# Performance work log

Hardware: AMD Instinct MI355X
Metric: run time of the kernel (lower is better)

The kernel has to match this reference:

```python
import jax, jax.numpy as jnp
import numpy as np

H = 8            # kv heads
R = 2            # qhead_ratio -> hq = 16 query heads
D = 128          # head_size
DEG = 2          # power degree
GATE_OFFSET = 6.906768  # ~log(999), gates start near 1


def setup_inputs() -> dict:
    key = jax.random.key(0)
    ks = jax.random.split(key, 7)
    B, T, C = 1, 2048, 2048
    q_dim = H * R * D   # 2048
    kv_dim = H * D      # 1024
    s = 0.02
    return {
        "hidden_states": jax.random.normal(ks[0], (B, T, C), dtype=jnp.float32),
        "Wq": jax.random.normal(ks[1], (C, q_dim), dtype=jnp.float32) * s,
        "Wk": jax.random.normal(ks[2], (C, kv_dim), dtype=jnp.float32) * s,
        "Wv": jax.random.normal(ks[3], (C, kv_dim), dtype=jnp.float32) * s,
        "Wg": jax.random.normal(ks[4], (C, H), dtype=jnp.float32) * s,
        "Wc": jax.random.normal(ks[5], (q_dim, C), dtype=jnp.float32) * s,
        "bc": jnp.zeros((C,), dtype=jnp.float32),
    }


def _power_attention(q, k, v, log_g):
    # q: [B,T,hq,D], k/v: [B,T,H,D], log_g: [B,T,H]
    B, T, hq, d = q.shape
    scale = 1.0 / d ** 0.5
    # GQA: query head i uses kv head i // R (q was viewed as (B,T,H,R,D))
    k = jnp.repeat(k, R, axis=2)            # [B,T,hq,D]
    v = jnp.repeat(v, R, axis=2)            # [B,T,hq,D]
    logG = jnp.cumsum(log_g, axis=1)        # [B,T,H]
    logG = jnp.repeat(logG, R, axis=2)      # [B,T,hq]
    logG = jnp.transpose(logG, (0, 2, 1))   # [B,hq,T]
    qk = jnp.einsum('bthd,bshd->bhts', q, k) * scale   # [B,hq,T,T]
    a = qk ** DEG                                       # even degree -> >= 0
    # gating decay exp(logG_t - logG_s) <= 1 for s <= t
    gate = logG[:, :, :, None] - logG[:, :, None, :]    # [B,hq,T,T]
    causal = jnp.tril(jnp.ones((T, T), dtype=bool))
    a = jnp.where(causal, a * jnp.exp(gate), 0.0)
    norm = jnp.sum(a, axis=-1) + 1e-6                   # [B,hq,T]
    y = jnp.einsum('bhts,bshd->bthd', a, v)             # [B,T,hq,D]
    y = y / jnp.transpose(norm, (0, 2, 1))[..., None]
    return y


def reference(hidden_states, Wq, Wk, Wv, Wg, Wc, bc):
    B, T, C = hidden_states.shape
    q = (hidden_states @ Wq).reshape(B, T, H * R, D)
    k = (hidden_states @ Wk).reshape(B, T, H, D)
    v = (hidden_states @ Wv).reshape(B, T, H, D)
    g = hidden_states @ Wg                              # [B,T,H]
    log_g = jax.nn.log_sigmoid(GATE_OFFSET + g.astype(jnp.float32))
    y = _power_attention(q, k, v, log_g)                # [B,T,hq,D]
    y = y.reshape(B, T, H * R * D)
    return y @ Wc + bc
```

## Files before the change

### kernel.cpp

```cpp
#include <hip/hip_runtime.h>

typedef unsigned short u16;
typedef unsigned int u32;
typedef unsigned long long u64;
typedef __bf16 bf16x8 __attribute__((ext_vector_type(8)));
typedef float f32x4 __attribute__((ext_vector_type(4)));

union FragAB {
  bf16x8 v;
  u16 u[8];
  u32 w[4];
  u64 d2[2];
};

__device__ __forceinline__ u16 f2bf(float f) {
  u32 u = __builtin_bit_cast(u32, f);
  u += 0x7fffu + ((u >> 16) & 1u);
  return (u16)(u >> 16);
}

__device__ __forceinline__ void gload_lds16(const void* g, void* l) {
  __builtin_amdgcn_global_load_lds((__attribute__((address_space(1))) void*)g,
                                   (__attribute__((address_space(3))) void*)l, 16, 0, 0);
}

__device__ __forceinline__ int permcol(int n) {
  int k = n & 31;
  return (n & ~31) | ((k & 12) << 1) | ((k & 16) >> 2) | (k & 3);
}

__global__ __launch_bounds__(256) void conv_perm_kernel(const float* __restrict__ in,
                                                        u16* __restrict__ out, int n4) {
  int i = blockIdx.x * 256 + threadIdx.x;
  if (i >= n4) return;
  float4 v = ((const float4*)in)[i];
  u64 pk = (u64)f2bf(v.x) | ((u64)f2bf(v.y) << 16) | ((u64)f2bf(v.z) << 32) |
           ((u64)f2bf(v.w) << 48);
  int col = (i << 2) & 2047;
  int g = (col >> 2) & 7;
  int ncol = (col & ~31) | ((2 * (g & 3) + (g >> 2)) << 2);
  size_t row = (size_t)(i >> 9);
  *(u64*)&out[row * 2048 + ncol] = pk;
}

__global__ __launch_bounds__(256) void tconv_kernel(const float* __restrict__ in,
                                                    u16* __restrict__ out, int K, int N) {
  __shared__ float tile[32][33];
  int col = threadIdx.x & 31;
  int row0 = threadIdx.x >> 5;
  int kb = blockIdx.y * 32, nb = blockIdx.x * 32;
  int pcol = permcol(col);
#pragma unroll
  for (int i = 0; i < 4; i++) {
    int r = row0 + i * 8;
    tile[r][col] = in[(size_t)(kb + r) * N + nb + col];
  }
  __syncthreads();
#pragma unroll
  for (int i = 0; i < 4; i++) {
    int r = row0 + i * 8;
    out[(size_t)(nb + r) * K + kb + pcol] = f2bf(tile[col][r]);
  }
}

__global__ __launch_bounds__(256) void tconv3_kernel(const float* __restrict__ Wq,
                                                     const float* __restrict__ Wk,
                                                     const float* __restrict__ Wv,
                                                     u16* __restrict__ slab) {
  __shared__ float tile[32][33];
  const int z = blockIdx.z;
  const float* src = (z < 2) ? Wq : (z == 2 ? Wk : Wv);
  const int srcN = (z < 2) ? 2048 : 1024;
  const int colBase = (z == 1) ? 1024 : 0;
  const int dstRowBase = z * 1024;
  int col = threadIdx.x & 31;
  int row0 = threadIdx.x >> 5;
  int kb = blockIdx.y * 32, nb = blockIdx.x * 32;
  int pcol = permcol(col);
#pragma unroll
  for (int i = 0; i < 4; i++) {
    int r = row0 + i * 8;
    tile[r][col] = src[(size_t)(kb + r) * srcN + colBase + nb + col];
  }
  __syncthreads();
#pragma unroll
  for (int i = 0; i < 4; i++) {
    int r = row0 + i * 8;
    slab[(size_t)(dstRowBase + nb + r) * 2048 + kb + pcol] = f2bf(tile[col][r]);
  }
}

__global__ __launch_bounds__(256) void gate_kernel(const float* __restrict__ hs,
                                                   const float* __restrict__ Wg,
                                                   float* __restrict__ lgt) {
  int lane = threadIdx.x & 63, wid = threadIdx.x >> 6;
  int t = blockIdx.x * 4 + wid;
  float acc[8] = {0.f, 0.f, 0.f, 0.f, 0.f, 0.f, 0.f, 0.f};
  for (int c = lane; c < 2048; c += 64) {
    float x = hs[(size_t)t * 2048 + c];
    float4 w0 = *(const float4*)&Wg[c * 8];
    float4 w1 = *(const float4*)&Wg[c * 8 + 4];
    acc[0] += x * w0.x; acc[1] += x * w0.y; acc[2] += x * w0.z; acc[3] += x * w0.w;
    acc[4] += x * w1.x; acc[5] += x * w1.y; acc[6] += x * w1.z; acc[7] += x * w1.w;
  }
#pragma unroll
  for (int h = 0; h < 8; h++) {
    float v = acc[h];
    for (int m = 1; m < 64; m <<= 1) v += __shfl_xor(v, m, 64);
    if (lane == 0) {
      float x = 6.906768f + v;
      lgt[h * 2048 + t] = -log1pf(__expf(-x));
    }
  }
}

__global__ __launch_bounds__(256) void cumsum_kernel(const float* __restrict__ lgt,
                                                     float* __restrict__ logG) {
  int h = blockIdx.x;
  __shared__ float buf[2048];
  for (int i = threadIdx.x; i < 2048; i += 256) buf[i] = lgt[h * 2048 + i];
  __syncthreads();
  for (int off = 1; off < 2048; off <<= 1) {
    float tmp[8];
#pragma unroll
    for (int j = 0; j < 8; j++) {
      int i = threadIdx.x + j * 256;
      tmp[j] = (i >= off) ? buf[i - off] : 0.f;
    }
    __syncthreads();
#pragma unroll
    for (int j = 0; j < 8; j++) {
      int i = threadIdx.x + j * 256;
      buf[i] += tmp[j];
    }
    __syncthreads();
  }
  for (int i = threadIdx.x; i < 2048; i += 256) logG[h * 2048 + i] = buf[i];
}

template <int MODE, int NT>
__global__ __launch_bounds__(512, 4) void gemm_v2(const u16* __restrict__ A,
                                                  const u16* __restrict__ BT,
                                                  void* __restrict__ C0,
                                                  void* __restrict__ C1,
                                                  int permLim) {
  __shared__ __align__(16) u16 As[2 * 128 * 64];
  __shared__ __align__(16) u16 Bs[2 * 128 * 64];
  constexpr int nwg = 16 * NT * (MODE == 2 ? 2 : 1);
  constexpr int cpx = nwg >> 3;
  const int raw = (int)blockIdx.x;
  const int wg = (raw & 7) * cpx + (raw >> 3);
  int bx, by, z;
  if constexpr (MODE == 2) {
    z = wg & 1;
    int t = wg >> 1;
    by = t >> 4;
    bx = t & 15;
  } else {
    z = 0;
    by = wg >> 4;
    bx = wg & 15;
  }
  const int kBeg = (MODE == 2) ? z * 1024 : 0;
  const int kEnd = (MODE == 2) ? kBeg + 1024 : 2048;
  constexpr int N = NT * 128;

  const int tid = threadIdx.x;
  const int lane = tid & 63, wid = tid >> 6;
  const int m0 = bx * 128, n0 = by * 128;
  const int wr = wid >> 2, wc = wid & 3;
  const int l15 = lane & 15, kg = lane >> 4;

  f32x4 acc[4][2];
#pragma unroll
  for (int i = 0; i < 4; i++)
#pragma unroll
    for (int j = 0; j < 2; j++) acc[i][j] = f32x4{0.f, 0.f, 0.f, 0.f};

  const int c0 = (wid * 2) * 64 + lane;
  const int c1 = c0 + 64;
  const int r0 = c0 >> 3, s0u = (c0 & 7) ^ (r0 & 7);
  const int r1 = c1 >> 3, s1u = (c1 & 7) ^ (r1 & 7);
  const u16* Asrc0 = A + (size_t)(m0 + r0) * 2048 + s0u * 8;
  const u16* Asrc1 = A + (size_t)(m0 + r1) * 2048 + s1u * 8;
  const u16* Bsrc0 = BT + (size_t)(n0 + r0) * 2048 + s0u * 8;
  const u16* Bsrc1 = BT + (size_t)(n0 + r1) * 2048 + s1u * 8;

  auto stage = [&](int buf, int k0) {
    u16* Ad = As + buf * 8192 + (wid * 2) * 512;
    u16* Bd = Bs + buf * 8192 + (wid * 2) * 512;
    gload_lds16(Asrc0 + k0, Ad);
    gload_lds16(Asrc1 + k0, Ad + 512);
    gload_lds16(Bsrc0 + k0, Bd);
    gload_lds16(Bsrc1 + k0, Bd + 512);
  };

  stage(0, kBeg);
  __syncthreads();

  int cur = 0;
  for (int k0 = kBeg; k0 < kEnd; k0 += 64) {
    if (k0 + 64 < kEnd) stage(cur ^ 1, k0 + 64);
    const u16* Ab = As + cur * 8192;
    const u16* Bb = Bs + cur * 8192;
#pragma unroll
    for (int ks = 0; ks < 2; ks++) {
      FragAB af[4], bfr[2];
#pragma unroll
      for (int mt = 0; mt < 4; mt++) {
        int row = wr * 64 + mt * 16 + l15;
        af[mt].v = *(const bf16x8*)&Ab[row * 64 + 8 * ((ks * 4 + kg) ^ (row & 7))];
      }
#pragma unroll
      for (int nt = 0; nt < 2; nt++) {
        int row = wc * 32 + nt * 16 + l15;
        bfr[nt].v = *(const bf16x8*)&Bb[row * 64 + 8 * ((ks * 4 + kg) ^ (row & 7))];
      }
#pragma unroll
      for (int mt = 0; mt < 4; mt++)
#pragma unroll
        for (int nt = 0; nt < 2; nt++)
          acc[mt][nt] = __builtin_amdgcn_mfma_f32_16x16x32_bf16(af[mt].v, bfr[nt].v, acc[mt][nt], 0, 0, 0);
    }
    __syncthreads();
    cur ^= 1;
  }

#pragma unroll
  for (int mt = 0; mt < 4; mt++) {
#pragma unroll
    for (int re = 0; re < 4; re++) {
      int m = m0 + wr * 64 + mt * 16 + kg * 4 + re;
#pragma unroll
      for (int nt = 0; nt < 2; nt++) {
        int n = n0 + wc * 32 + nt * 16 + l15;
        float v = acc[mt][nt][re];
        if constexpr (MODE == 2) {
          float* P = z ? (float*)C1 : (float*)C0;
          P[(size_t)m * N + n] = v;
        } else {
          int nw = (n < permLim) ? permcol(n) : n;
          ((u16*)C0)[(size_t)m * N + nw] = f2bf(v);
        }
      }
    }
  }
}

__global__ __launch_bounds__(256, 2) void power_attn(const u16* __restrict__ QKV,
                                                     const float* __restrict__ logG,
                                                     float* __restrict__ y0p,
                                                     float* __restrict__ y1p,
                                                     float* __restrict__ npart) {
  __shared__ __align__(16) u16 Ks[2 * 64 * 128];
  __shared__ __align__(16) u16 Vt[2 * 128 * 64];
  __shared__ float eS[2 * 64];

  const int raw = (int)blockIdx.x;
  const int orig = (raw & 7) * 64 + (raw >> 3);
  const int hq = orig >> 5;
  const int j_ = orig & 31;
  const int half = j_ & 1;
  const int bslot = j_ >> 1;
  const int qa = (bslot + (hq >> 1) * 3) & 15;
  const int qt = (hq & 1) ? (15 - qa) : qa;
  const int hk = hq >> 1;
  const int t0 = qt * 128;

  const int tid = threadIdx.x, lane = tid & 63, wid = tid >> 6;
  const int l15 = lane & 15, kg = lane >> 4;
  const int l7 = l15 & 7;

  const int s4 = tid & 15, dgrp = tid >> 4;
  const int ubase = 4 * (s4 >> 3) + (s4 & 3);
  const int vhb = (s4 >> 2) & 1;

  const u16* Kbase = QKV + 2048 + hk * 128;
  const u16* Vbase = QKV + 3072 + hk * 128 + dgrp * 8;
  const float* lgh = logG + hk * 2048;

  FragAB qf[2][4];
  float celg[2];
  int myT[2];
  const float scale2 = 0.0078125f;
#pragma unroll
  for (int cg = 0; cg < 2; cg++) {
    myT[cg] = t0 + wid * 16 + cg * 64 + l15;
    const u16* qrow = QKV + (size_t)myT[cg] * 4096 + hq * 128;
#pragma unroll
    for (int ks = 0; ks < 4; ks++) qf[cg][ks].v = *(const bf16x8*)(qrow + ks * 32 + kg * 8);
    celg[cg] = scale2 * __expf(lgh[myT[cg]]);
  }

  f32x4 yacc[8][2];
#pragma unroll
  for (int i = 0; i < 8; i++)
#pragma unroll
    for (int c = 0; c < 2; c++) yacc[i][c] = f32x4{0.f, 0.f, 0.f, 0.f};
  float nacc[2] = {0.f, 0.f};

  const int itBeg = half ? (qt + 1) : 0;
  const int itEnd = half ? (2 * qt + 2) : (qt + 1);

  auto stageK = [&](int s0, int bb) {
#pragma unroll
    for (int c = 0; c < 4; c++) {
      int ch = (wid * 4 + c) * 64 + lane;
      int row = ch >> 4, du = ch & 15;
      int su = du ^ (row & 7);
      gload_lds16(Kbase + (size_t)(s0 + row) * 4096 + su * 8, &Ks[bb * 8192 + (wid * 4 + c) * 512]);
    }
  };
  auto loadV = [&](int s0, uint4* vr) {
#pragma unroll
    for (int r = 0; r < 4; r++) vr[r] = *(const uint4*)(Vbase + (size_t)(s0 + 4 * s4 + r) * 4096);
  };
  auto writeV = [&](int bb, const uint4* vr) {
    u16* vd = &Vt[bb * 8192];
    const u32* w0 = (const u32*)&vr[0];
    const u32* w1 = (const u32*)&vr[1];
    const u32* w2 = (const u32*)&vr[2];
    const u32* w3 = (const u32*)&vr[3];
#pragma unroll
    for (int i = 0; i < 8; i++) {
      u32 sel = (i & 1) ? 0x07060302u : 0x05040100u;
      u32 lo = __builtin_amdgcn_perm(w1[i >> 1], w0[i >> 1], sel);
      u32 hi = __builtin_amdgcn_perm(w3[i >> 1], w2[i >> 1], sel);
      int d = dgrp * 8 + i;
      int e = d * 64 + 8 * (ubase ^ i) + 4 * vhb;
      *(u64*)&vd[e] = (u64)lo | ((u64)hi << 32);
    }
  };

  {
    uint4 vr[4];
    stageK(itBeg * 64, 0);
    loadV(itBeg * 64, vr);
    float ee = (tid < 64) ? lgh[itBeg * 64 + tid] : 0.f;
    writeV(0, vr);
    if (tid < 64) eS[tid] = __expf(-ee);
  }
  __syncthreads();

  for (int it = itBeg; it < itEnd; it++) {
    const int cur = (it - itBeg) & 1;
    const int s0 = it * 64;
    const bool hasNext = (it + 1 < itEnd);
    uint4 vr[4];
    float ee = 0.f;
    if (hasNext) {
      stageK(s0 + 64, cur ^ 1);
      loadV(s0 + 64, vr);
      if (tid < 64) ee = lgh[s0 + 64 + tid];
    }

    const u16* kb = &Ks[cur * 8192];
    f32x4 sacc[4][2];
#pragma unroll
    for (int mt = 0; mt < 4; mt++)
#pragma unroll
      for (int cg = 0; cg < 2; cg++) sacc[mt][cg] = f32x4{0.f, 0.f, 0.f, 0.f};
    __builtin_amdgcn_s_setprio(1);
#pragma unroll
    for (int ks = 0; ks < 4; ks++) {
#pragma unroll
      for (int mt = 0; mt < 4; mt++) {
        FragAB af;
        af.v = *(const bf16x8*)&kb[(mt * 16 + l15) * 128 + 8 * ((4 * ks + kg) ^ l7)];
        sacc[mt][0] = __builtin_amdgcn_mfma_f32_16x16x32_bf16(af.v, qf[0][ks].v, sacc[mt][0], 0, 0, 0);
        sacc[mt][1] = __builtin_amdgcn_mfma_f32_16x16x32_bf16(af.v, qf[1][ks].v, sacc[mt][1], 0, 0, 0);
      }
    }
    __builtin_amdgcn_s_setprio(0);

    FragAB pa[2][2];
    const bool need_mask = (it >= 2 * qt);
#pragma unroll
    for (int mt = 0; mt < 4; mt++) {
      f32x4 ev = *(const f32x4*)&eS[cur * 64 + mt * 16 + kg * 4];
#pragma unroll
      for (int cg = 0; cg < 2; cg++) {
        u32 pb[4];
#pragma unroll
        for (int r = 0; r < 4; r++) {
          float x = sacc[mt][cg][r];
          float p = x * x * celg[cg] * ev[r];
          if (need_mask) {
            int s = s0 + mt * 16 + kg * 4 + r;
            p = (s <= myT[cg]) ? p : 0.f;
          }
          nacc[cg] += p;
          pb[r] = __builtin_bit_cast(u32, p) + 0x8000u;
        }
        pa[cg][mt >> 1].w[(mt & 1) * 2 + 0] = __builtin_amdgcn_perm(pb[1], pb[0], 0x07060302u);
        pa[cg][mt >> 1].w[(mt & 1) * 2 + 1] = __builtin_amdgcn_perm(pb[3], pb[2], 0x07060302u);
      }
    }

    const u16* vb = &Vt[cur * 8192];
    const int x0 = 8 * (kg ^ l7);
    __builtin_amdgcn_s_setprio(1);
#pragma unroll
    for (int ksv = 0; ksv < 2; ksv++) {
      const int xo = x0 ^ (ksv * 32);
#pragma unroll
      for (int nt = 0; nt < 8; nt++) {
        FragAB bfv;
        bfv.v = *(const bf16x8*)&vb[(nt * 16 + l15) * 64 + xo];
        yacc[nt][0] = __builtin_amdgcn_mfma_f32_16x16x32_bf16(pa[0][ksv].v, bfv.v, yacc[nt][0], 0, 0, 0);
        yacc[nt][1] = __builtin_amdgcn_mfma_f32_16x16x32_bf16(pa[1][ksv].v, bfv.v, yacc[nt][1], 0, 0, 0);
      }
    }
    __builtin_amdgcn_s_setprio(0);

    if (hasNext) {
      writeV(cur ^ 1, vr);
      if (tid < 64) eS[(cur ^ 1) * 64 + tid] = __expf(-ee);
    }
    __syncthreads();
  }

  float* yp = half ? y1p : y0p;
  float* np = npart + half * (16 * 2048);
#pragma unroll
  for (int cg = 0; cg < 2; cg++) {
    float nf = nacc[cg];
    nf += __shfl_xor(nf, 16, 64);
    nf += __shfl_xor(nf, 32, 64);
    if (lane < 16) np[hq * 2048 + t0 + wid * 16 + cg * 64 + lane] = nf;
#pragma unroll
    for (int re = 0; re < 4; re++) {
      int trow = t0 + wid * 16 + cg * 64 + kg * 4 + re;
      float* yrow = yp + (size_t)trow * 2048 + hq * 128;
#pragma unroll
      for (int nt = 0; nt < 8; nt++) yrow[nt * 16 + l15] = yacc[nt][cg][re];
    }
  }
}

__global__ __launch_bounds__(256) void combine_kernel(const float* __restrict__ y0,
                                                      const float* __restrict__ y1,
                                                      const float* __restrict__ npart,
                                                      u16* __restrict__ yb) {
  int i = blockIdx.x * 256 + threadIdx.x;
  int e0 = i << 2;
  int t = e0 >> 11;
  int hq = (e0 >> 7) & 15;
  float nn = npart[hq * 2048 + t] + npart[32768 + hq * 2048 + t] + 1e-6f;
  float inv = 1.0f / nn;
  float4 a = ((const float4*)y0)[i];
  float4 b = ((const float4*)y1)[i];
  u64 pk = (u64)f2bf((a.x + b.x) * inv) | ((u64)f2bf((a.y + b.y) * inv) << 16) |
           ((u64)f2bf((a.z + b.z) * inv) << 32) | ((u64)f2bf((a.w + b.w) * inv) << 48);
  int col = e0 & 2047;
  int g = (col >> 2) & 7;
  int ncol = (col & ~31) | ((2 * (g & 3) + (g >> 2)) << 2);
  *(u64*)&yb[(size_t)t * 2048 + ncol] = pk;
}

__global__ __launch_bounds__(256) void combine2_kernel(const float* __restrict__ p0,
                                                       float* __restrict__ out,
                                                       const float* __restrict__ bias) {
  int i = blockIdx.x * 256 + threadIdx.x;
  int col = (i << 2) & 2047;
  float4 a = ((const float4*)p0)[i];
  float4 b = ((const float4*)out)[i];
  float4 bb = *(const float4*)&bias[col];
  float4 r;
  r.x = a.x + b.x + bb.x;
  r.y = a.y + b.y + bb.y;
  r.z = a.z + b.z + bb.z;
  r.w = a.w + b.w + bb.w;
  ((float4*)out)[i] = r;
}

extern "C" void kernel_launch(void* const* d_in, const int* in_sizes, int n_in,
                              void* d_out, int out_size, void* d_ws, size_t ws_size,
                              hipStream_t stream) {
  (void)in_sizes; (void)n_in; (void)out_size; (void)ws_size;
  const float* hs = (const float*)d_in[0];
  const float* Wq = (const float*)d_in[1];
  const float* Wk = (const float*)d_in[2];
  const float* Wv = (const float*)d_in[3];
  const float* Wg = (const float*)d_in[4];
  const float* Wc = (const float*)d_in[5];
  const float* bc = (const float*)d_in[6];
  float* out = (float*)d_out;

  char* ws = (char*)d_ws;
  const size_t MB = 1024 * 1024;
  u16* slab   = (u16*)(ws);
  u16* hs_bf  = (u16*)(ws + 16 * MB);
  u16* qkv_bf = (u16*)(ws + 24 * MB);
  float* y0p  = (float*)(ws + 40 * MB);
  float* npart = (float*)(ws + 56 * MB);
  float* lgt  = (float*)(ws + 56 * MB + 262144);
  float* logG = (float*)(ws + 56 * MB + 327680);
  float* y1p = out;
  u16* y_bf = hs_bf;
  u16* WcT = slab;

  conv_perm_kernel<<<4096, 256, 0, stream>>>(hs, hs_bf, 2048 * 2048 / 4);
  tconv3_kernel<<<dim3(32, 64, 4), 256, 0, stream>>>(Wq, Wk, Wv, slab);

  gemm_v2<1, 32><<<512, 512, 0, stream>>>(hs_bf, slab, qkv_bf, nullptr, 3072);

  gate_kernel<<<512, 256, 0, stream>>>(hs, Wg, lgt);
  cumsum_kernel<<<8, 256, 0, stream>>>(lgt, logG);

  tconv_kernel<<<dim3(64, 64), 256, 0, stream>>>(Wc, WcT, 2048, 2048);

  power_attn<<<dim3(512), 256, 0, stream>>>(qkv_bf, logG, y0p, y1p, npart);
  combine_kernel<<<4096, 256, 0, stream>>>(y0p, y1p, npart, y_bf);

  gemm_v2<2, 16><<<512, 512, 0, stream>>>(y_bf, WcT, y0p, out, 0);
  combine2_kernel<<<4096, 256, 0, stream>>>(y0p, out, bc);
}
```

Measured before the change: 164.2 us.

## Split attention KV range into four quarters with smaller tiles and bf16 partials

Power attention now splits each query tile's causal KV range into four chunks instead of two, using 32-row KV tiles, a padded V layout and 3 blocks per CU, so 1024 blocks launch instead of 512. Three of the four partial outputs are stored as bf16 to reduce write and read traffic, and the combine kernel sums four partials. The weight transpose kernels move to 64x64 tiles with fewer blocks. The cost is more partial-sum traffic, one more combine input, and some precision loss from storing partials in bf16.

```diff
diff --git a/kernel.cpp b/kernel.cpp
--- a/kernel.cpp
+++ b/kernel.cpp
@@ -45,20 +45,20 @@
 
 __global__ __launch_bounds__(256) void tconv_kernel(const float* __restrict__ in,
                                                     u16* __restrict__ out, int K, int N) {
-  __shared__ float tile[32][33];
-  int col = threadIdx.x & 31;
-  int row0 = threadIdx.x >> 5;
-  int kb = blockIdx.y * 32, nb = blockIdx.x * 32;
+  __shared__ float tile[64][65];
+  int col = threadIdx.x & 63;
+  int r0 = threadIdx.x >> 6;
+  int kb = blockIdx.y * 64, nb = blockIdx.x * 64;
   int pcol = permcol(col);
 #pragma unroll
-  for (int i = 0; i < 4; i++) {
-    int r = row0 + i * 8;
+  for (int i = 0; i < 16; i++) {
+    int r = r0 + i * 4;
     tile[r][col] = in[(size_t)(kb + r) * N + nb + col];
   }
   __syncthreads();
 #pragma unroll
-  for (int i = 0; i < 4; i++) {
-    int r = row0 + i * 8;
+  for (int i = 0; i < 16; i++) {
+    int r = r0 + i * 4;
     out[(size_t)(nb + r) * K + kb + pcol] = f2bf(tile[col][r]);
   }
 }
@@ -67,25 +67,25 @@
                                                      const float* __restrict__ Wk,
                                                      const float* __restrict__ Wv,
                                                      u16* __restrict__ slab) {
-  __shared__ float tile[32][33];
   const int z = blockIdx.z;
-  const float* src = (z < 2) ? Wq : (z == 2 ? Wk : Wv);
-  const int srcN = (z < 2) ? 2048 : 1024;
-  const int colBase = (z == 1) ? 1024 : 0;
-  const int dstRowBase = z * 1024;
-  int col = threadIdx.x & 31;
-  int row0 = threadIdx.x >> 5;
-  int kb = blockIdx.y * 32, nb = blockIdx.x * 32;
+  if (z > 0 && blockIdx.x >= 16) return;
+  __shared__ float tile[64][65];
+  const float* src = (z == 0) ? Wq : (z == 1 ? Wk : Wv);
+  const int srcN = (z == 0) ? 2048 : 1024;
+  const int dstRowBase = (z == 0) ? 0 : (z == 1 ? 2048 : 3072);
+  int col = threadIdx.x & 63;
+  int r0 = threadIdx.x >> 6;
+  int kb = blockIdx.y * 64, nb = blockIdx.x * 64;
   int pcol = permcol(col);
 #pragma unroll
-  for (int i = 0; i < 4; i++) {
-    int r = row0 + i * 8;
-    tile[r][col] = src[(size_t)(kb + r) * srcN + colBase + nb + col];
+  for (int i = 0; i < 16; i++) {
+    int r = r0 + i * 4;
+    tile[r][col] = src[(size_t)(kb + r) * srcN + nb + col];
   }
   __syncthreads();
 #pragma unroll
-  for (int i = 0; i < 4; i++) {
-    int r = row0 + i * 8;
+  for (int i = 0; i < 16; i++) {
+    int r = r0 + i * 4;
     slab[(size_t)(dstRowBase + nb + r) * 2048 + kb + pcol] = f2bf(tile[col][r]);
   }
 }
@@ -247,33 +247,31 @@
   }
 }
 
-__global__ __launch_bounds__(256, 2) void power_attn(const u16* __restrict__ QKV,
+__global__ __launch_bounds__(256, 3) void power_attn(const u16* __restrict__ QKV,
                                                      const float* __restrict__ logG,
-                                                     float* __restrict__ y0p,
+                                                     u16* __restrict__ y0b,
                                                      float* __restrict__ y1p,
+                                                     u16* __restrict__ y2b,
+                                                     u16* __restrict__ y3b,
                                                      float* __restrict__ npart) {
-  __shared__ __align__(16) u16 Ks[2 * 64 * 128];
-  __shared__ __align__(16) u16 Vt[2 * 128 * 64];
-  __shared__ float eS[2 * 64];
+  __shared__ __align__(16) u16 Ks[2 * 32 * 128];
+  __shared__ __align__(16) u16 Vt[2 * 128 * 40];
+  __shared__ float eS[2 * 32];
 
   const int raw = (int)blockIdx.x;
-  const int orig = (raw & 7) * 64 + (raw >> 3);
-  const int hq = orig >> 5;
-  const int j_ = orig & 31;
-  const int half = j_ & 1;
-  const int bslot = j_ >> 1;
-  const int qa = (bslot + (hq >> 1) * 3) & 15;
-  const int qt = (hq & 1) ? (15 - qa) : qa;
+  const int orig = (raw & 7) * 128 + (raw >> 3);
+  const int hq = orig >> 6;
+  const int j_ = orig & 63;
+  const int quarter = j_ >> 4;
+  const int slot = j_ & 15;
+  const int qt = (quarter < 2) ? slot : (15 - slot);
   const int hk = hq >> 1;
   const int t0 = qt * 128;
 
   const int tid = threadIdx.x, lane = tid & 63, wid = tid >> 6;
   const int l15 = lane & 15, kg = lane >> 4;
   const int l7 = l15 & 7;
-
   const int s4 = tid & 15, dgrp = tid >> 4;
-  const int ubase = 4 * (s4 >> 3) + (s4 & 3);
-  const int vhb = (s4 >> 2) & 1;
 
   const u16* Kbase = QKV + 2048 + hk * 128;
   const u16* Vbase = QKV + 3072 + hk * 128 + dgrp * 8;
@@ -299,72 +297,69 @@
     for (int c = 0; c < 2; c++) yacc[i][c] = f32x4{0.f, 0.f, 0.f, 0.f};
   float nacc[2] = {0.f, 0.f};
 
-  const int itBeg = half ? (qt + 1) : 0;
-  const int itEnd = half ? (2 * qt + 2) : (qt + 1);
+  const int itBeg = quarter * (qt + 1);
+  const int itEnd = itBeg + (qt + 1);
 
   auto stageK = [&](int s0, int bb) {
 #pragma unroll
-    for (int c = 0; c < 4; c++) {
-      int ch = (wid * 4 + c) * 64 + lane;
+    for (int c = 0; c < 2; c++) {
+      int ch = (wid * 2 + c) * 64 + lane;
       int row = ch >> 4, du = ch & 15;
       int su = du ^ (row & 7);
-      gload_lds16(Kbase + (size_t)(s0 + row) * 4096 + su * 8, &Ks[bb * 8192 + (wid * 4 + c) * 512]);
+      gload_lds16(Kbase + (size_t)(s0 + row) * 4096 + su * 8, &Ks[bb * 4096 + (wid * 2 + c) * 512]);
     }
   };
   auto loadV = [&](int s0, uint4* vr) {
-#pragma unroll
-    for (int r = 0; r < 4; r++) vr[r] = *(const uint4*)(Vbase + (size_t)(s0 + 4 * s4 + r) * 4096);
+    vr[0] = *(const uint4*)(Vbase + (size_t)(s0 + 2 * s4) * 4096);
+    vr[1] = *(const uint4*)(Vbase + (size_t)(s0 + 2 * s4 + 1) * 4096);
   };
   auto writeV = [&](int bb, const uint4* vr) {
-    u16* vd = &Vt[bb * 8192];
+    u16* vd = &Vt[bb * 5120];
     const u32* w0 = (const u32*)&vr[0];
     const u32* w1 = (const u32*)&vr[1];
-    const u32* w2 = (const u32*)&vr[2];
-    const u32* w3 = (const u32*)&vr[3];
+    int e = 8 * ((s4 >> 1) & 3) + 4 * (s4 >> 3) + 2 * (s4 & 1);
 #pragma unroll
     for (int i = 0; i < 8; i++) {
       u32 sel = (i & 1) ? 0x07060302u : 0x05040100u;
-      u32 lo = __builtin_amdgcn_perm(w1[i >> 1], w0[i >> 1], sel);
-      u32 hi = __builtin_amdgcn_perm(w3[i >> 1], w2[i >> 1], sel);
+      u32 val = __builtin_amdgcn_perm(w1[i >> 1], w0[i >> 1], sel);
       int d = dgrp * 8 + i;
-      int e = d * 64 + 8 * (ubase ^ i) + 4 * vhb;
-      *(u64*)&vd[e] = (u64)lo | ((u64)hi << 32);
+      *(u32*)&vd[d * 40 + e] = val;
     }
   };
 
   {
-    uint4 vr[4];
-    stageK(itBeg * 64, 0);
-    loadV(itBeg * 64, vr);
-    float ee = (tid < 64) ? lgh[itBeg * 64 + tid] : 0.f;
+    uint4 vr[2];
+    stageK(itBeg * 32, 0);
+    loadV(itBeg * 32, vr);
+    float ee = (tid < 32) ? lgh[itBeg * 32 + tid] : 0.f;
     writeV(0, vr);
-    if (tid < 64) eS[tid] = __expf(-ee);
+    if (tid < 32) eS[tid] = __expf(-ee);
   }
   __syncthreads();
 
   for (int it = itBeg; it < itEnd; it++) {
     const int cur = (it - itBeg) & 1;
-    const int s0 = it * 64;
+    const int s0 = it * 32;
     const bool hasNext = (it + 1 < itEnd);
-    uint4 vr[4];
+    uint4 vr[2];
     float ee = 0.f;
     if (hasNext) {
-      stageK(s0 + 64, cur ^ 1);
-      loadV(s0 + 64, vr);
-      if (tid < 64) ee = lgh[s0 + 64 + tid];
-    }
-
-    const u16* kb = &Ks[cur * 8192];
-    f32x4 sacc[4][2];
-#pragma unroll
-    for (int mt = 0; mt < 4; mt++)
+      stageK(s0 + 32, cur ^ 1);
+      loadV(s0 + 32, vr);
+      if (tid < 32) ee = lgh[s0 + 32 + tid];
+    }
+
+    const u16* kb = &Ks[cur * 4096];
+    f32x4 sacc[2][2];
+#pragma unroll
+    for (int mt = 0; mt < 2; mt++)
 #pragma unroll
       for (int cg = 0; cg < 2; cg++) sacc[mt][cg] = f32x4{0.f, 0.f, 0.f, 0.f};
     __builtin_amdgcn_s_setprio(1);
 #pragma unroll
     for (int ks = 0; ks < 4; ks++) {
 #pragma unroll
-      for (int mt = 0; mt < 4; mt++) {
+      for (int mt = 0; mt < 2; mt++) {
         FragAB af;
         af.v = *(const bf16x8*)&kb[(mt * 16 + l15) * 128 + 8 * ((4 * ks + kg) ^ l7)];
         sacc[mt][0] = __builtin_amdgcn_mfma_f32_16x16x32_bf16(af.v, qf[0][ks].v, sacc[mt][0], 0, 0, 0);
@@ -373,14 +368,13 @@
     }
     __builtin_amdgcn_s_setprio(0);
 
-    FragAB pa[2][2];
-    const bool need_mask = (it >= 2 * qt);
-#pragma unroll
-    for (int mt = 0; mt < 4; mt++) {
-      f32x4 ev = *(const f32x4*)&eS[cur * 64 + mt * 16 + kg * 4];
+    FragAB pa[2];
+    const bool need_mask = (it >= 4 * qt);
+#pragma unroll
+    for (int mt = 0; mt < 2; mt++) {
+      f32x4 ev = *(const f32x4*)&eS[cur * 32 + mt * 16 + kg * 4];
 #pragma unroll
       for (int cg = 0; cg < 2; cg++) {
-        u32 pb[4];
 #pragma unroll
         for (int r = 0; r < 4; r++) {
           float x = sacc[mt][cg][r];
@@ -390,38 +384,30 @@
             p = (s <= myT[cg]) ? p : 0.f;
           }
           nacc[cg] += p;
-          pb[r] = __builtin_bit_cast(u32, p) + 0x8000u;
+          pa[cg].u[mt * 4 + r] = f2bf(p);
         }
-        pa[cg][mt >> 1].w[(mt & 1) * 2 + 0] = __builtin_amdgcn_perm(pb[1], pb[0], 0x07060302u);
-        pa[cg][mt >> 1].w[(mt & 1) * 2 + 1] = __builtin_amdgcn_perm(pb[3], pb[2], 0x07060302u);
       }
     }
 
-    const u16* vb = &Vt[cur * 8192];
-    const int x0 = 8 * (kg ^ l7);
+    const u16* vb = &Vt[cur * 5120];
     __builtin_amdgcn_s_setprio(1);
 #pragma unroll
-    for (int ksv = 0; ksv < 2; ksv++) {
-      const int xo = x0 ^ (ksv * 32);
-#pragma unroll
-      for (int nt = 0; nt < 8; nt++) {
-        FragAB bfv;
-        bfv.v = *(const bf16x8*)&vb[(nt * 16 + l15) * 64 + xo];
-        yacc[nt][0] = __builtin_amdgcn_mfma_f32_16x16x32_bf16(pa[0][ksv].v, bfv.v, yacc[nt][0], 0, 0, 0);
-        yacc[nt][1] = __builtin_amdgcn_mfma_f32_16x16x32_bf16(pa[1][ksv].v, bfv.v, yacc[nt][1], 0, 0, 0);
-      }
+    for (int nt = 0; nt < 8; nt++) {
+      FragAB bfv;
+      bfv.v = *(const bf16x8*)&vb[(nt * 16 + l15) * 40 + 8 * kg];
+      yacc[nt][0] = __builtin_amdgcn_mfma_f32_16x16x32_bf16(pa[0].v, bfv.v, yacc[nt][0], 0, 0, 0);
+      yacc[nt][1] = __builtin_amdgcn_mfma_f32_16x16x32_bf16(pa[1].v, bfv.v, yacc[nt][1], 0, 0, 0);
     }
     __builtin_amdgcn_s_setprio(0);
 
     if (hasNext) {
       writeV(cur ^ 1, vr);
-      if (tid < 64) eS[(cur ^ 1) * 64 + tid] = __expf(-ee);
+      if (tid < 32) eS[(cur ^ 1) * 32 + tid] = __expf(-ee);
     }
     __syncthreads();
   }
 
-  float* yp = half ? y1p : y0p;
-  float* np = npart + half * (16 * 2048);
+  float* np = npart + quarter * (16 * 2048);
 #pragma unroll
   for (int cg = 0; cg < 2; cg++) {
     float nf = nacc[cg];
@@ -431,27 +417,47 @@
 #pragma unroll
     for (int re = 0; re < 4; re++) {
       int trow = t0 + wid * 16 + cg * 64 + kg * 4 + re;
-      float* yrow = yp + (size_t)trow * 2048 + hq * 128;
-#pragma unroll
-      for (int nt = 0; nt < 8; nt++) yrow[nt * 16 + l15] = yacc[nt][cg][re];
-    }
-  }
-}
-
-__global__ __launch_bounds__(256) void combine_kernel(const float* __restrict__ y0,
+      size_t base = (size_t)trow * 2048 + hq * 128;
+      if (quarter == 1) {
+#pragma unroll
+        for (int nt = 0; nt < 8; nt++) y1p[base + nt * 16 + l15] = yacc[nt][cg][re];
+      } else {
+        u16* yb = (quarter == 0) ? y0b : (quarter == 2 ? y2b : y3b);
+#pragma unroll
+        for (int nt = 0; nt < 8; nt++) yb[base + nt * 16 + l15] = f2bf(yacc[nt][cg][re]);
+      }
+    }
+  }
+}
+
+__global__ __launch_bounds__(256) void combine_kernel(const u16* __restrict__ y0b,
                                                       const float* __restrict__ y1,
+                                                      const u16* __restrict__ y2b,
+                                                      const u16* __restrict__ y3b,
                                                       const float* __restrict__ npart,
                                                       u16* __restrict__ yb) {
   int i = blockIdx.x * 256 + threadIdx.x;
   int e0 = i << 2;
   int t = e0 >> 11;
   int hq = (e0 >> 7) & 15;
-  float nn = npart[hq * 2048 + t] + npart[32768 + hq * 2048 + t] + 1e-6f;
+  int nidx = hq * 2048 + t;
+  float nn = npart[nidx] + npart[32768 + nidx] + npart[65536 + nidx] + npart[98304 + nidx] + 1e-6f;
   float inv = 1.0f / nn;
-  float4 a = ((const float4*)y0)[i];
+  u64 a0 = *(const u64*)&y0b[e0];
   float4 b = ((const float4*)y1)[i];
-  u64 pk = (u64)f2bf((a.x + b.x) * inv) | ((u64)f2bf((a.y + b.y) * inv) << 16) |
-           ((u64)f2bf((a.z + b.z) * inv) << 32) | ((u64)f2bf((a.w + b.w) * inv) << 48);
+  u64 a2 = *(const u64*)&y2b[e0];
+  u64 a3 = *(const u64*)&y3b[e0];
+  float r[4];
+#pragma unroll
+  for (int j = 0; j < 4; j++) {
+    float v0 = __builtin_bit_cast(float, (u32)((a0 >> (16 * j)) & 0xffffu) << 16);
+    float v2 = __builtin_bit_cast(float, (u32)((a2 >> (16 * j)) & 0xffffu) << 16);
+    float v3 = __builtin_bit_cast(float, (u32)((a3 >> (16 * j)) & 0xffffu) << 16);
+    float bj = (j == 0) ? b.x : (j == 1) ? b.y : (j == 2) ? b.z : b.w;
+    r[j] = (v0 + bj + v2 + v3) * inv;
+  }
+  u64 pk = (u64)f2bf(r[0]) | ((u64)f2bf(r[1]) << 16) | ((u64)f2bf(r[2]) << 32) |
+           ((u64)f2bf(r[3]) << 48);
   int col = e0 & 2047;
   int g = (col >> 2) & 7;
   int ncol = (col & ~31) | ((2 * (g & 3) + (g >> 2)) << 2);
@@ -490,28 +496,31 @@
   char* ws = (char*)d_ws;
   const size_t MB = 1024 * 1024;
   u16* slab   = (u16*)(ws);
+  float* lgt  = (float*)(ws + 8 * MB);
+  float* logG = (float*)(ws + 8 * MB + 65536);
+  float* npart = (float*)(ws + 8 * MB + 131072);
   u16* hs_bf  = (u16*)(ws + 16 * MB);
+  u16* y3b    = (u16*)(ws + 16 * MB);
   u16* qkv_bf = (u16*)(ws + 24 * MB);
+  u16* y_bf   = (u16*)(ws + 24 * MB);
+  u16* y0b    = (u16*)(ws + 40 * MB);
+  u16* y2b    = (u16*)(ws + 48 * MB);
   float* y0p  = (float*)(ws + 40 * MB);
-  float* npart = (float*)(ws + 56 * MB);
-  float* lgt  = (float*)(ws + 56 * MB + 262144);
-  float* logG = (float*)(ws + 56 * MB + 327680);
   float* y1p = out;
-  u16* y_bf = hs_bf;
   u16* WcT = slab;
 
   conv_perm_kernel<<<4096, 256, 0, stream>>>(hs, hs_bf, 2048 * 2048 / 4);
-  tconv3_kernel<<<dim3(32, 64, 4), 256, 0, stream>>>(Wq, Wk, Wv, slab);
+  tconv3_kernel<<<dim3(32, 32, 3), 256, 0, stream>>>(Wq, Wk, Wv, slab);
 
   gemm_v2<1, 32><<<512, 512, 0, stream>>>(hs_bf, slab, qkv_bf, nullptr, 3072);
 
   gate_kernel<<<512, 256, 0, stream>>>(hs, Wg, lgt);
   cumsum_kernel<<<8, 256, 0, stream>>>(lgt, logG);
 
-  tconv_kernel<<<dim3(64, 64), 256, 0, stream>>>(Wc, WcT, 2048, 2048);
-
-  power_attn<<<dim3(512), 256, 0, stream>>>(qkv_bf, logG, y0p, y1p, npart);
-  combine_kernel<<<4096, 256, 0, stream>>>(y0p, y1p, npart, y_bf);
+  tconv_kernel<<<dim3(32, 32), 256, 0, stream>>>(Wc, WcT, 2048, 2048);
+
+  power_attn<<<dim3(1024), 256, 0, stream>>>(qkv_bf, logG, y0b, y1p, y2b, y3b, npart);
+  combine_kernel<<<4096, 256, 0, stream>>>(y0b, y1p, y2b, y3b, npart, y_bf);
 
   gemm_v2<2, 16><<<512, 512, 0, stream>>>(y_bf, WcT, y0p, out, 0);
   combine2_kernel<<<4096, 256, 0, stream>>>(y0p, out, bc);
```

New measurement: 167.6 us. 1.02x slower.
